# Optimization experiments

Hardware: AMD Instinct MI355X
Metric: run time of the kernel (lower is better)

Reference implementation:

```python
import jax, jax.numpy as jnp
import numpy as np

DIM = 192          # out_dim
HEADS = 8          # num_heads (split into 2 branches of 4)
SS = (4, 8)        # split_size
B, HH, WW, CIN = 8, 128, 128, 192


def calc_mask(H, W, wh, ww):
    # Swin-style shift mask for windows of (wh, ww), shift (wh//2, ww//2).
    sh, sw = wh // 2, ww // 2
    h = jnp.arange(H)
    w = jnp.arange(W)
    hreg = (h >= H - wh).astype(jnp.int32) + (h >= H - sh).astype(jnp.int32)
    wreg = (w >= W - ww).astype(jnp.int32) + (w >= W - sw).astype(jnp.int32)
    img = hreg[:, None] * 3 + wreg[None, :]                      # (H, W) region ids
    win = img.reshape(H // wh, wh, W // ww, ww).transpose(0, 2, 1, 3).reshape(-1, wh * ww)
    return jnp.where(win[:, :, None] != win[:, None, :], -100.0, 0.0)  # (nW, N, N)


def window_attention(q, k, v, mask, d, Hsp, Wsp):
    # q,k,v: (B, C, H, W); mask: (u*v, N, N); d heads, window Hsp x Wsp
    Bc, C, H, W = k.shape
    u, vv = H // Hsp, W // Wsp
    c = C // d
    N = Hsp * Wsp
    scale = c ** -0.5

    def v2w(t):  # 'b (d c) (u h) (v w) -> (b u v) d (h w) c'
        return t.reshape(Bc, d, c, u, Hsp, vv, Wsp).transpose(0, 3, 5, 1, 4, 6, 2).reshape(Bc * u * vv, d, N, c)

    qw, kw, vw = v2w(q), v2w(k), v2w(v)
    attn = jnp.einsum('ndic,ndjc->ndij', qw, kw) * scale          # (B*u*v, d, N, N)
    attn = attn.reshape(Bc, u * vv, d, N, N) + mask[None, :, None, :, :]
    a = jax.nn.softmax(attn, axis=-1).reshape(Bc * u * vv, d, N, N)
    o = jnp.einsum('ndij,ndjc->ndic', a, vw)
    # '(b u v) d (h w) c -> b (d c) (u h) (v w)'
    return o.reshape(Bc, u, vv, d, Hsp, Wsp, c).transpose(0, 3, 6, 1, 4, 2, 5).reshape(Bc, C, H, W)


def setup_inputs() -> dict:
    key = jax.random.key(0)
    k0, k1, k2, k3 = jax.random.split(key, 4)
    x = jax.random.normal(k0, (B, HH * WW, CIN), dtype=jnp.float32)
    Wq = jax.random.normal(k1, (CIN, DIM), dtype=jnp.float32) * 0.02
    Wkv = jax.random.normal(k2, (CIN, 2 * DIM), dtype=jnp.float32) * 0.02
    Wproj = jax.random.normal(k3, (DIM, DIM), dtype=jnp.float32) * 0.02
    bproj = jnp.zeros((DIM,), dtype=jnp.float32)
    return {"x": x, "Wq": Wq, "Wkv": Wkv, "Wproj": Wproj, "bproj": bproj, "H": HH, "W": WW}


def reference(x, Wq, Wkv, Wproj, bproj, H, W):
    Bc, L, _ = x.shape
    C = Wq.shape[1]
    q = (x @ Wq).reshape(Bc, H, W, C).transpose(0, 3, 1, 2)       # (B, C, H, W)
    kv = (x @ Wkv).reshape(Bc, H, W, 2, C)
    k = kv[..., 0, :].transpose(0, 3, 1, 2)
    v = kv[..., 1, :].transpose(0, 3, 1, 2)

    Ch = C // 2
    s0, s1 = SS[0] // 2, SS[1] // 2
    roll0 = lambda t: jnp.roll(t, (-s0, -s1), axis=(-2, -1))
    roll1 = lambda t: jnp.roll(t, (-s1, -s0), axis=(-2, -1))
    mask0 = calc_mask(H, W, SS[0], SS[1])   # branch 0: 4x8 windows
    mask1 = calc_mask(H, W, SS[1], SS[0])   # branch 1: 8x4 windows
    d = HEADS // 2

    x0 = window_attention(roll0(q[:, :Ch]), roll0(k[:, :Ch]), roll0(v[:, :Ch]), mask0, d, SS[0], SS[1])
    x1 = window_attention(roll1(q[:, Ch:]), roll1(k[:, Ch:]), roll1(v[:, Ch:]), mask1, d, SS[1], SS[0])
    x0 = jnp.roll(x0, (s0, s1), axis=(-2, -1))
    x1 = jnp.roll(x1, (s1, s0), axis=(-2, -1))

    out = jnp.concatenate([x0, x1], axis=1)                        # (B, C, H, W)
    out = out.transpose(0, 2, 3, 1).reshape(Bc, L, C)
    return out @ Wproj + bproj
```

## Files before the change

kernel.cpp:

```cpp
#include <hip/hip_runtime.h>
#include <hip/hip_bf16.h>
#include <stdint.h>

typedef __bf16 bf16;
typedef __bf16 bf16x8 __attribute__((ext_vector_type(8)));
typedef __bf16 bf16x4 __attribute__((ext_vector_type(4)));
typedef float  f32x4  __attribute__((ext_vector_type(4)));

#define MROWS 131072

__device__ __forceinline__ f32x4 mfma16(bf16x8 a, bf16x8 b, f32x4 c) {
    return __builtin_amdgcn_mfma_f32_16x16x32_bf16(a, b, c, 0, 0, 0);
}
__device__ __forceinline__ f32x4 zero4() {
    f32x4 z; z[0]=0.f; z[1]=0.f; z[2]=0.f; z[3]=0.f; return z;
}
__device__ __forceinline__ bf16x8 zero8() {
    bf16x8 z;
#pragma unroll
    for (int i = 0; i < 8; ++i) z[i] = (bf16)0.f;
    return z;
}
template <int CTRL>
__device__ __forceinline__ float rowror(float x) {
    return __int_as_float(
        __builtin_amdgcn_mov_dpp(__float_as_int(x), CTRL, 0xF, 0xF, false));
}
__device__ __forceinline__ float rowsum16(float s) {
    s += rowror<0x128>(s);
    s += rowror<0x124>(s);
    s += rowror<0x122>(s);
    s += rowror<0x121>(s);
    return s;
}

__global__ void kw_transpose(const float* __restrict__ Wq, const float* __restrict__ Wkv,
                             const float* __restrict__ Wp, bf16* __restrict__ Wt,
                             bf16* __restrict__ Wpt) {
    int col = blockIdx.x;
    int k = threadIdx.x;
    if (col < 192)      Wt[col * 192 + k] = (bf16)Wq[k * 192 + col];
    else if (col < 576) Wt[col * 192 + k] = (bf16)Wkv[k * 384 + (col - 192)];
    else                Wpt[(col - 576) * 192 + k] = (bf16)Wp[k * 192 + (col - 576)];
}

__global__ __launch_bounds__(256, 4) void kfused(const float* __restrict__ X,
                                                 const bf16* __restrict__ Wt,
                                                 bf16* __restrict__ Out) {
    const int bid = blockIdx.x;
    const int slab = bid & 7;
    const int t = bid >> 3;
    const int img = t >> 7;
    const int idx = t & 127;
    int branch, wa, wb;
    if (idx < 64) {
        branch = 0; wa = slab * 4 + (idx >> 4); wb = idx & 15;
    } else {
        branch = 1; int j = idx - 64; wa = slab * 2 + (j >> 5); wb = j & 31;
    }
    const int wh = branch ? 8 : 4, ww = branch ? 4 : 8;
    const int lww = branch ? 2 : 3;
    const int sh = wh >> 1, sw = ww >> 1;

    __shared__ __align__(16) char smem[31232];
    bf16 (*xs)[200]    = (bf16(*)[200])smem;
    bf16 (*qs)[104]    = (bf16(*)[104])smem;
    bf16 (*ob)[104]    = (bf16(*)[104])smem;
    bf16 (*kss)[104]   = (bf16(*)[104])(smem + 6656);
    bf16 (*pl)[32][40] = (bf16(*)[32][40])(smem + 13312);
    bf16 (*vt)[40]     = (bf16(*)[40])(smem + 23552);
    __shared__ int pix[32];
    __shared__ int rid[32];

    const int tid = threadIdx.x;
    const int hd = tid >> 6;
    const int l = tid & 63, li = l & 15, lk = l >> 4;

    if (tid < 32) {
        int ih = tid >> lww, iw = tid & (ww - 1);
        int hh = wa * wh + ih, wp = wb * ww + iw;
        int hreg = (hh >= 128 - wh) + (hh >= 128 - sh);
        int wreg = (wp >= 128 - ww) + (wp >= 128 - sw);
        rid[tid] = hreg * 3 + wreg;
        int srh = (hh + sh) & 127, srw = (wp + sw) & 127;
        pix[tid] = img * 16384 + srh * 128 + srw;
    }

#pragma unroll
    for (int i = 0; i < 3; ++i) {
        int c = tid + i * 256;
        int row = c / 24, col8 = (c % 24) * 8;
        int ih = row >> lww, iw = row & (ww - 1);
        int hh = wa * wh + ih, wp = wb * ww + iw;
        int srh = (hh + sh) & 127, srw = (wp + sw) & 127;
        const float* p = X + (size_t)(img * 16384 + srh * 128 + srw) * 192 + col8;
        f32x4 f0 = *(const f32x4*)p;
        f32x4 f1 = *(const f32x4*)(p + 4);
        bf16x8 v;
#pragma unroll
        for (int e = 0; e < 4; ++e) { v[e] = (bf16)f0[e]; v[4 + e] = (bf16)f1[e]; }
        *(bf16x8*)&xs[row][col8] = v;
    }
    __syncthreads();

    bf16x8 xf[2][6];
#pragma unroll
    for (int mt = 0; mt < 2; ++mt)
#pragma unroll
        for (int ks = 0; ks < 6; ++ks)
            xf[mt][ks] = *(const bf16x8*)&xs[mt * 16 + li][ks * 32 + lk * 8];

#define LOADW(dst, nt) {                                                            \
        int seg_ = (nt) / 6, cwi_ = ((nt) % 6) * 16;                                \
        const bf16* wr = Wt + (size_t)(seg_ * 192 + branch * 96 + cwi_ + li) * 192  \
                            + lk * 8;                                               \
        _Pragma("unroll")                                                           \
        for (int ks = 0; ks < 6; ++ks) dst[ks] = *(const bf16x8*)(wr + ks * 32);    \
    }
#define MFMA_SCATTER(frag, nt) {                                                    \
        f32x4 a0 = zero4(), a1 = zero4();                                           \
        _Pragma("unroll")                                                           \
        for (int ks = 0; ks < 6; ++ks) {                                            \
            a0 = mfma16(frag[ks], xf[0][ks], a0);                                   \
            a1 = mfma16(frag[ks], xf[1][ks], a1);                                   \
        }                                                                           \
        int seg_ = (nt) / 6, cwi_ = ((nt) % 6) * 16;                                \
        if (seg_ < 2) {                                                             \
            bf16 (*dst)[104] = (seg_ == 0) ? qs : kss;                              \
            bf16x4 p0, p1;                                                          \
            _Pragma("unroll")                                                       \
            for (int r = 0; r < 4; ++r) { p0[r] = (bf16)a0[r]; p1[r] = (bf16)a1[r]; } \
            *(bf16x4*)&dst[li][cwi_ + lk * 4] = p0;                                 \
            *(bf16x4*)&dst[16 + li][cwi_ + lk * 4] = p1;                            \
        } else {                                                                    \
            _Pragma("unroll")                                                       \
            for (int r = 0; r < 4; ++r) {                                           \
                int vc = cwi_ + lk * 4 + r;                                         \
                vt[vc][li] = (bf16)a0[r];                                           \
                vt[vc][16 + li] = (bf16)a1[r];                                      \
            }                                                                       \
        }                                                                           \
    }

    bf16x8 cur[6], nxt[6];
    LOADW(cur, hd);
    __syncthreads();

#pragma unroll
    for (int j = 0; j < 4; ++j) {
        int nt = hd + 4 * j;
        if (j < 3) {
            LOADW(nxt, nt + 4);
        } else if (hd < 2) {
            LOADW(nxt, nt + 4);
        }
        MFMA_SCATTER(cur, nt);
#pragma unroll
        for (int ks = 0; ks < 6; ++ks) cur[ks] = nxt[ks];
    }
    if (hd < 2) {
        MFMA_SCATTER(cur, hd + 16);
    }
    __syncthreads();

    bf16x8 aq[2], bk[2];
#pragma unroll
    for (int t2 = 0; t2 < 2; ++t2) {
        if (lk < 3) {
            aq[t2] = *(const bf16x8*)&qs[t2 * 16 + li][hd * 24 + lk * 8];
            bk[t2] = *(const bf16x8*)&kss[t2 * 16 + li][hd * 24 + lk * 8];
        } else {
            aq[t2] = zero8();
            bk[t2] = zero8();
        }
    }
    f32x4 s[2][2];
#pragma unroll
    for (int it = 0; it < 2; ++it)
#pragma unroll
        for (int jt = 0; jt < 2; ++jt) s[it][jt] = mfma16(aq[it], bk[jt], zero4());

    const float scale = 0.2041241452319315f;
    const int r0 = lk * 4;
    const int rj0 = rid[li], rj1 = rid[16 + li];
    float inv_[2][4];
#pragma unroll
    for (int it = 0; it < 2; ++it) {
#pragma unroll
        for (int r = 0; r < 4; ++r) {
            int i = it * 16 + r0 + r;
            int ri = rid[i];
            float v0 = s[it][0][r] * scale + ((ri != rj0) ? -100.f : 0.f);
            float v1 = s[it][1][r] * scale + ((ri != rj1) ? -100.f : 0.f);
            float e0 = __expf(v0), e1 = __expf(v1);
            pl[hd][i][li] = (bf16)e0;
            pl[hd][i][16 + li] = (bf16)e1;
            float sm = rowsum16(e0 + e1);
            inv_[it][r] = 1.f / sm;
        }
    }
    __syncthreads();

    bf16x8 ap[2], bv[2];
#pragma unroll
    for (int it = 0; it < 2; ++it)
        ap[it] = *(const bf16x8*)&pl[hd][it * 16 + li][lk * 8];
#pragma unroll
    for (int ct = 0; ct < 2; ++ct) {
        int col = ct * 16 + li;
        if (col > 23) col = 23;
        bv[ct] = *(const bf16x8*)&vt[hd * 24 + col][lk * 8];
    }
    f32x4 o[2][2];
#pragma unroll
    for (int it = 0; it < 2; ++it)
#pragma unroll
        for (int ct = 0; ct < 2; ++ct) o[it][ct] = mfma16(ap[it], bv[ct], zero4());

#pragma unroll
    for (int it = 0; it < 2; ++it)
#pragma unroll
        for (int ct = 0; ct < 2; ++ct) {
            int col = ct * 16 + li;
            if (col < 24) {
#pragma unroll
                for (int r = 0; r < 4; ++r)
                    ob[it * 16 + r0 + r][hd * 24 + col] =
                        (bf16)(o[it][ct][r] * inv_[it][r]);
            }
        }
    __syncthreads();
    for (int c = tid; c < 384; c += 256) {
        int row = c / 12, ch = c % 12;
        *(bf16x8*)(Out + (size_t)pix[row] * 192 + branch * 96 + ch * 8) =
            *(const bf16x8*)&ob[row][ch * 8];
    }
#undef LOADW
#undef MFMA_SCATTER
}

#define BSTR 200
__global__ __launch_bounds__(256, 4) void kproj(const bf16* __restrict__ Ab,
                                                const bf16* __restrict__ Wpt,
                                                const float* __restrict__ bias,
                                                float* __restrict__ Out) {
    __shared__ __align__(16) bf16 Bs[96][BSTR];
    const int lid = blockIdx.x;
    const int xcd = lid & 7, s = lid >> 3;
    const int mg = xcd * 128 + s / 2;
    const int nb = s & 1;
    const int tid = threadIdx.x;
    const int w = tid >> 6, l = tid & 63, li = l & 15, lk = l >> 4;
    const int rb = mg * 128 + w * 32;
    const int cb = nb * 96;

    bf16x8 a[2][6];
#pragma unroll
    for (int it = 0; it < 2; ++it)
#pragma unroll
        for (int ks = 0; ks < 6; ++ks)
            a[it][ks] = *(const bf16x8*)(Ab + (size_t)(rb + it * 16 + li) * 192 + ks * 32 + lk * 8);

#pragma unroll
    for (int i = 0; i < 9; ++i) {
        int c = i * 256 + tid;
        int r = c / 24, col = (c % 24) * 8;
        *(bf16x8*)&Bs[r][col] = *(const bf16x8*)(Wpt + (size_t)(cb + r) * 192 + col);
    }
    __syncthreads();

    f32x4 acc[2][6];
#pragma unroll
    for (int it = 0; it < 2; ++it)
#pragma unroll
        for (int nt = 0; nt < 6; ++nt) acc[it][nt] = zero4();

#pragma unroll
    for (int nt = 0; nt < 6; ++nt) {
#pragma unroll
        for (int ks = 0; ks < 6; ++ks) {
            bf16x8 b = *(const bf16x8*)&Bs[nt * 16 + li][ks * 32 + lk * 8];
            acc[0][nt] = mfma16(b, a[0][ks], acc[0][nt]);
            acc[1][nt] = mfma16(b, a[1][ks], acc[1][nt]);
        }
    }

#pragma unroll
    for (int nt = 0; nt < 6; ++nt) {
        f32x4 bv4 = *(const f32x4*)(bias + cb + nt * 16 + lk * 4);
#pragma unroll
        for (int it = 0; it < 2; ++it) {
            f32x4 ov = acc[it][nt];
#pragma unroll
            for (int r = 0; r < 4; ++r) ov[r] += bv4[r];
            *(f32x4*)(Out + (size_t)(rb + it * 16 + li) * 192 + cb + nt * 16 + lk * 4) = ov;
        }
    }
}

extern "C" void kernel_launch(void* const* d_in, const int* in_sizes, int n_in,
                              void* d_out, int out_size, void* d_ws, size_t ws_size,
                              hipStream_t stream) {
    const float* x    = (const float*)d_in[0];
    const float* Wq   = (const float*)d_in[1];
    const float* Wkv  = (const float*)d_in[2];
    const float* Wp   = (const float*)d_in[3];
    const float* bias = (const float*)d_in[4];
    float* out = (float*)d_out;

    bf16* Ab  = (bf16*)d_ws;
    bf16* Wt  = Ab + (size_t)MROWS * 192;
    bf16* Wpt = Wt + 576 * 192;

    hipLaunchKernelGGL(kw_transpose, dim3(768), dim3(192), 0, stream, Wq, Wkv, Wp, Wt, Wpt);
    hipLaunchKernelGGL(kfused, dim3(8192), dim3(256), 0, stream, x, Wt, Ab);
    hipLaunchKernelGGL(kproj, dim3(2048), dim3(256), 0, stream, Ab, Wpt, bias, out);
}
```

Baseline: 145.2 us.

## Split each window block across 8 waves, one 16-row half per wave

The fused attention kernel now launches 512 threads per window block instead of 256, with each head's work split between two waves that each own 16 of the 32 window rows. Each wave keeps half as many X fragments and accumulators, and the software double-buffered weight prefetch is replaced by a single buffer reloaded after each MFMA group. This is meant to cut per-thread register pressure and add latency-hiding parallelism. The cost is that every wave reloads the full weight fragments from global memory, doubling weight traffic, and there are twice as many waves contending for barriers.

```diff
diff --git a/kernel.cpp b/kernel.cpp
--- a/kernel.cpp
+++ b/kernel.cpp
@@ -44,7 +44,7 @@
     else                Wpt[(col - 576) * 192 + k] = (bf16)Wp[k * 192 + (col - 576)];
 }
 
-__global__ __launch_bounds__(256, 4) void kfused(const float* __restrict__ X,
+__global__ __launch_bounds__(512, 4) void kfused(const float* __restrict__ X,
                                                  const bf16* __restrict__ Wt,
                                                  bf16* __restrict__ Out) {
     const int bid = blockIdx.x;
@@ -73,7 +73,9 @@
     __shared__ int rid[32];
 
     const int tid = threadIdx.x;
-    const int hd = tid >> 6;
+    const int wv = tid >> 6;
+    const int hd = wv & 3;
+    const int half = wv >> 2;
     const int l = tid & 63, li = l & 15, lk = l >> 4;
 
     if (tid < 32) {
@@ -86,29 +88,28 @@
         pix[tid] = img * 16384 + srh * 128 + srw;
     }
 
-#pragma unroll
-    for (int i = 0; i < 3; ++i) {
-        int c = tid + i * 256;
-        int row = c / 24, col8 = (c % 24) * 8;
-        int ih = row >> lww, iw = row & (ww - 1);
-        int hh = wa * wh + ih, wp = wb * ww + iw;
-        int srh = (hh + sh) & 127, srw = (wp + sw) & 127;
-        const float* p = X + (size_t)(img * 16384 + srh * 128 + srw) * 192 + col8;
-        f32x4 f0 = *(const f32x4*)p;
-        f32x4 f1 = *(const f32x4*)(p + 4);
-        bf16x8 v;
-#pragma unroll
-        for (int e = 0; e < 4; ++e) { v[e] = (bf16)f0[e]; v[4 + e] = (bf16)f1[e]; }
-        *(bf16x8*)&xs[row][col8] = v;
-    }
-    __syncthreads();
-
-    bf16x8 xf[2][6];
-#pragma unroll
-    for (int mt = 0; mt < 2; ++mt)
-#pragma unroll
-        for (int ks = 0; ks < 6; ++ks)
-            xf[mt][ks] = *(const bf16x8*)&xs[mt * 16 + li][ks * 32 + lk * 8];
+#define XCHUNK(c) {                                                                 \
+        int row = (c) / 24, col8 = ((c) % 24) * 8;                                  \
+        int ih = row >> lww, iw = row & (ww - 1);                                   \
+        int hh = wa * wh + ih, wp = wb * ww + iw;                                   \
+        int srh = (hh + sh) & 127, srw = (wp + sw) & 127;                           \
+        const float* p = X + (size_t)(img * 16384 + srh * 128 + srw) * 192 + col8;  \
+        f32x4 f0 = *(const f32x4*)p;                                                \
+        f32x4 f1 = *(const f32x4*)(p + 4);                                          \
+        bf16x8 v;                                                                   \
+        _Pragma("unroll")                                                           \
+        for (int e = 0; e < 4; ++e) { v[e] = (bf16)f0[e]; v[4 + e] = (bf16)f1[e]; } \
+        *(bf16x8*)&xs[row][col8] = v;                                               \
+    }
+    XCHUNK(tid);
+    if (tid < 256) XCHUNK(512 + tid);
+#undef XCHUNK
+    __syncthreads();
+
+    bf16x8 xf[6];
+#pragma unroll
+    for (int ks = 0; ks < 6; ++ks)
+        xf[ks] = *(const bf16x8*)&xs[half * 16 + li][ks * 32 + lk * 8];
 
 #define LOADW(dst, nt) {                                                            \
         int seg_ = (nt) / 6, cwi_ = ((nt) % 6) * 16;                                \
@@ -117,126 +118,92 @@
         _Pragma("unroll")                                                           \
         for (int ks = 0; ks < 6; ++ks) dst[ks] = *(const bf16x8*)(wr + ks * 32);    \
     }
-#define MFMA_SCATTER(frag, nt) {                                                    \
-        f32x4 a0 = zero4(), a1 = zero4();                                           \
-        _Pragma("unroll")                                                           \
-        for (int ks = 0; ks < 6; ++ks) {                                            \
-            a0 = mfma16(frag[ks], xf[0][ks], a0);                                   \
-            a1 = mfma16(frag[ks], xf[1][ks], a1);                                   \
-        }                                                                           \
-        int seg_ = (nt) / 6, cwi_ = ((nt) % 6) * 16;                                \
-        if (seg_ < 2) {                                                             \
-            bf16 (*dst)[104] = (seg_ == 0) ? qs : kss;                              \
-            bf16x4 p0, p1;                                                          \
-            _Pragma("unroll")                                                       \
-            for (int r = 0; r < 4; ++r) { p0[r] = (bf16)a0[r]; p1[r] = (bf16)a1[r]; } \
-            *(bf16x4*)&dst[li][cwi_ + lk * 4] = p0;                                 \
-            *(bf16x4*)&dst[16 + li][cwi_ + lk * 4] = p1;                            \
-        } else {                                                                    \
-            _Pragma("unroll")                                                       \
-            for (int r = 0; r < 4; ++r) {                                           \
-                int vc = cwi_ + lk * 4 + r;                                         \
-                vt[vc][li] = (bf16)a0[r];                                           \
-                vt[vc][16 + li] = (bf16)a1[r];                                      \
-            }                                                                       \
-        }                                                                           \
-    }
-
-    bf16x8 cur[6], nxt[6];
+
+    bf16x8 cur[6];
     LOADW(cur, hd);
     __syncthreads();
 
 #pragma unroll
-    for (int j = 0; j < 4; ++j) {
+    for (int j = 0; j < 5; ++j) {
         int nt = hd + 4 * j;
-        if (j < 3) {
-            LOADW(nxt, nt + 4);
-        } else if (hd < 2) {
-            LOADW(nxt, nt + 4);
-        }
-        MFMA_SCATTER(cur, nt);
-#pragma unroll
-        for (int ks = 0; ks < 6; ++ks) cur[ks] = nxt[ks];
-    }
-    if (hd < 2) {
-        MFMA_SCATTER(cur, hd + 16);
-    }
-    __syncthreads();
-
-    bf16x8 aq[2], bk[2];
-#pragma unroll
-    for (int t2 = 0; t2 < 2; ++t2) {
-        if (lk < 3) {
-            aq[t2] = *(const bf16x8*)&qs[t2 * 16 + li][hd * 24 + lk * 8];
-            bk[t2] = *(const bf16x8*)&kss[t2 * 16 + li][hd * 24 + lk * 8];
+        if (j == 4 && hd >= 2) break;
+        f32x4 a0 = zero4();
+#pragma unroll
+        for (int ks = 0; ks < 6; ++ks) a0 = mfma16(cur[ks], xf[ks], a0);
+        if (j < 3 || (j == 3 && hd < 2)) LOADW(cur, nt + 4);
+        int seg_ = nt / 6, cwi_ = (nt % 6) * 16;
+        if (seg_ < 2) {
+            bf16 (*dst)[104] = (seg_ == 0) ? qs : kss;
+            bf16x4 p0;
+#pragma unroll
+            for (int r = 0; r < 4; ++r) p0[r] = (bf16)a0[r];
+            *(bf16x4*)&dst[half * 16 + li][cwi_ + lk * 4] = p0;
         } else {
-            aq[t2] = zero8();
-            bk[t2] = zero8();
-        }
-    }
-    f32x4 s[2][2];
-#pragma unroll
-    for (int it = 0; it < 2; ++it)
-#pragma unroll
-        for (int jt = 0; jt < 2; ++jt) s[it][jt] = mfma16(aq[it], bk[jt], zero4());
+#pragma unroll
+            for (int r = 0; r < 4; ++r)
+                vt[cwi_ + lk * 4 + r][half * 16 + li] = (bf16)a0[r];
+        }
+    }
+    __syncthreads();
+
+    bf16x8 aq, bk[2];
+    if (lk < 3) {
+        aq = *(const bf16x8*)&qs[half * 16 + li][hd * 24 + lk * 8];
+        bk[0] = *(const bf16x8*)&kss[li][hd * 24 + lk * 8];
+        bk[1] = *(const bf16x8*)&kss[16 + li][hd * 24 + lk * 8];
+    } else {
+        aq = zero8(); bk[0] = zero8(); bk[1] = zero8();
+    }
+    f32x4 s[2];
+#pragma unroll
+    for (int jt = 0; jt < 2; ++jt) s[jt] = mfma16(aq, bk[jt], zero4());
 
     const float scale = 0.2041241452319315f;
     const int r0 = lk * 4;
     const int rj0 = rid[li], rj1 = rid[16 + li];
-    float inv_[2][4];
-#pragma unroll
-    for (int it = 0; it < 2; ++it) {
-#pragma unroll
-        for (int r = 0; r < 4; ++r) {
-            int i = it * 16 + r0 + r;
-            int ri = rid[i];
-            float v0 = s[it][0][r] * scale + ((ri != rj0) ? -100.f : 0.f);
-            float v1 = s[it][1][r] * scale + ((ri != rj1) ? -100.f : 0.f);
-            float e0 = __expf(v0), e1 = __expf(v1);
-            pl[hd][i][li] = (bf16)e0;
-            pl[hd][i][16 + li] = (bf16)e1;
-            float sm = rowsum16(e0 + e1);
-            inv_[it][r] = 1.f / sm;
-        }
-    }
-    __syncthreads();
-
-    bf16x8 ap[2], bv[2];
-#pragma unroll
-    for (int it = 0; it < 2; ++it)
-        ap[it] = *(const bf16x8*)&pl[hd][it * 16 + li][lk * 8];
+    float inv_[4];
+#pragma unroll
+    for (int r = 0; r < 4; ++r) {
+        int i = half * 16 + r0 + r;
+        int ri = rid[i];
+        float v0 = s[0][r] * scale + ((ri != rj0) ? -100.f : 0.f);
+        float v1 = s[1][r] * scale + ((ri != rj1) ? -100.f : 0.f);
+        float e0 = __expf(v0), e1 = __expf(v1);
+        pl[hd][i][li] = (bf16)e0;
+        pl[hd][i][16 + li] = (bf16)e1;
+        float sm = rowsum16(e0 + e1);
+        inv_[r] = 1.f / sm;
+    }
+    __syncthreads();
+
+    bf16x8 ap = *(const bf16x8*)&pl[hd][half * 16 + li][lk * 8];
+    bf16x8 bv[2];
 #pragma unroll
     for (int ct = 0; ct < 2; ++ct) {
         int col = ct * 16 + li;
         if (col > 23) col = 23;
         bv[ct] = *(const bf16x8*)&vt[hd * 24 + col][lk * 8];
     }
-    f32x4 o[2][2];
-#pragma unroll
-    for (int it = 0; it < 2; ++it)
-#pragma unroll
-        for (int ct = 0; ct < 2; ++ct) o[it][ct] = mfma16(ap[it], bv[ct], zero4());
-
-#pragma unroll
-    for (int it = 0; it < 2; ++it)
-#pragma unroll
-        for (int ct = 0; ct < 2; ++ct) {
-            int col = ct * 16 + li;
-            if (col < 24) {
-#pragma unroll
-                for (int r = 0; r < 4; ++r)
-                    ob[it * 16 + r0 + r][hd * 24 + col] =
-                        (bf16)(o[it][ct][r] * inv_[it][r]);
-            }
-        }
-    __syncthreads();
-    for (int c = tid; c < 384; c += 256) {
-        int row = c / 12, ch = c % 12;
+    f32x4 o[2];
+#pragma unroll
+    for (int ct = 0; ct < 2; ++ct) o[ct] = mfma16(ap, bv[ct], zero4());
+
+#pragma unroll
+    for (int ct = 0; ct < 2; ++ct) {
+        int col = ct * 16 + li;
+        if (col < 24) {
+#pragma unroll
+            for (int r = 0; r < 4; ++r)
+                ob[half * 16 + r0 + r][hd * 24 + col] = (bf16)(o[ct][r] * inv_[r]);
+        }
+    }
+    __syncthreads();
+    if (tid < 384) {
+        int row = tid / 12, ch = tid % 12;
         *(bf16x8*)(Out + (size_t)pix[row] * 192 + branch * 96 + ch * 8) =
             *(const bf16x8*)&ob[row][ch * 8];
     }
 #undef LOADW
-#undef MFMA_SCATTER
 }
 
 #define BSTR 200
@@ -313,6 +280,6 @@
     bf16* Wpt = Wt + 576 * 192;
 
     hipLaunchKernelGGL(kw_transpose, dim3(768), dim3(192), 0, stream, Wq, Wkv, Wp, Wt, Wpt);
-    hipLaunchKernelGGL(kfused, dim3(8192), dim3(256), 0, stream, x, Wt, Ab);
+    hipLaunchKernelGGL(kfused, dim3(8192), dim3(512), 0, stream, x, Wt, Ab);
     hipLaunchKernelGGL(kproj, dim3(2048), dim3(256), 0, stream, Ab, Wpt, bias, out);
 }
```

Measured after the change: 236.4 us. +62.8%, slower.
